# Kernel optimization log

Hardware: AMD Instinct MI355X
Metric: run time of the kernel (lower is better)

Reference implementation:

```python
import jax, jax.numpy as jnp
import numpy as np

N = 100000
E = 1600000
C_IN = 128
H = 128
C_OUT = 128
DEPTH = 3
RATIO = 0.5
EPS = 1e-5


def gcn_conv(x, W, b, src, dst, mask, n):
    # PyG GCNConv: out = D^-1/2 (A+I) D^-1/2 (x @ W) + b, masked edges dropped
    h = x @ W  # [n, out]
    ew = mask.astype(h.dtype)  # [E]
    deg = 1.0 + jax.ops.segment_sum(ew, dst, num_segments=n)  # self-loop included
    dinv = jax.lax.rsqrt(deg)
    norm = dinv[src] * dinv[dst] * ew  # [E]
    agg = jax.ops.segment_sum(h[src] * norm[:, None], dst, num_segments=n)
    agg = agg + h * (1.0 / deg)[:, None]  # self-loop contribution
    return agg + b


def bn_train(x, g, beta):
    # BatchNorm1d training forward: biased variance over nodes
    m = jnp.mean(x, axis=0)
    v = jnp.mean((x - m) ** 2, axis=0)
    return (x - m) * jax.lax.rsqrt(v + EPS) * g + beta


def topk_pool(x, w, src, dst, mask, k):
    # score = tanh(x.w / ||w||); keep top-k nodes, relabel edges, mask invalid ones
    score = jnp.tanh((x * w).sum(-1) / jnp.sqrt((w * w).sum()))
    _, idx = jax.lax.top_k(score, k)
    n = x.shape[0]
    new_id = jnp.zeros((n,), jnp.int32).at[idx].set(jnp.arange(k, dtype=jnp.int32))
    kept = jnp.zeros((n,), bool).at[idx].set(True)
    mask2 = mask & kept[src] & kept[dst]
    return x[idx], new_id[src], new_id[dst], mask2, idx


def setup_inputs() -> dict:
    key = jax.random.key(0)
    ks = jax.random.split(key, 16)
    sc_in = 1.0 / np.sqrt(C_IN)
    sc_h = 1.0 / np.sqrt(H)
    sc_2h = 1.0 / np.sqrt(2 * H)
    return {
        "x": jax.random.normal(ks[0], (N, C_IN), jnp.float32),
        "edge_index": jax.random.randint(ks[1], (2, E), 0, N, dtype=jnp.int32),
        "in_W": jax.random.normal(ks[2], (C_IN, H), jnp.float32) * sc_in,
        "in_b": jnp.zeros((H,), jnp.float32),
        "dn_W": jax.random.normal(ks[3], (DEPTH, H, H), jnp.float32) * sc_h,
        "dn_b": jnp.zeros((DEPTH, H), jnp.float32),
        "dn_g": jnp.ones((DEPTH, H), jnp.float32),
        "dn_beta": jnp.zeros((DEPTH, H), jnp.float32),
        "pool_w": jax.random.normal(ks[4], (DEPTH, H), jnp.float32),
        "bot_W": jax.random.normal(ks[5], (H, H), jnp.float32) * sc_h,
        "bot_b": jnp.zeros((H,), jnp.float32),
        "up_W": jax.random.normal(ks[6], (DEPTH, 2 * H, H), jnp.float32) * sc_2h,
        "up_b": jnp.zeros((DEPTH, H), jnp.float32),
        "up_g": jnp.ones((DEPTH, H), jnp.float32),
        "up_beta": jnp.zeros((DEPTH, H), jnp.float32),
        "out_W": jax.random.normal(ks[7], (H, C_OUT), jnp.float32) * sc_h,
        "out_b": jnp.zeros((C_OUT,), jnp.float32),
    }


def reference(x, edge_index, in_W, in_b, dn_W, dn_b, dn_g, dn_beta, pool_w,
              bot_W, bot_b, up_W, up_b, up_g, up_beta, out_W, out_b):
    src, dst = edge_index[0], edge_index[1]
    mask = jnp.ones((src.shape[0],), bool)
    n = x.shape[0]
    x = gcn_conv(x, in_W, in_b, src, dst, mask, n)
    xs, stack = [], []
    for i in range(DEPTH):
        x = gcn_conv(x, dn_W[i], dn_b[i], src, dst, mask, n)
        x = jax.nn.relu(bn_train(x, dn_g[i], dn_beta[i]))
        xs.append(x)
        k = int(RATIO * n)
        x2, src2, dst2, mask2, idx = topk_pool(x, pool_w[i], src, dst, mask, k)
        stack.append((src, dst, mask, idx, n))
        x, src, dst, mask, n = x2, src2, dst2, mask2, k
    x = jax.nn.relu(gcn_conv(x, bot_W, bot_b, src, dst, mask, n))
    for i in range(DEPTH):
        psrc, pdst, pmask, idx, pn = stack[DEPTH - 1 - i]
        xf = jnp.zeros((pn, x.shape[1]), x.dtype).at[idx].set(x)  # unpool zero-scatter
        src, dst, mask, n = psrc, pdst, pmask, pn
        x = jnp.concatenate([xf, xs[DEPTH - 1 - i]], axis=1)  # [pn, 2H]
        x = gcn_conv(x, up_W[i], up_b[i], src, dst, mask, n)
        x = jax.nn.relu(bn_train(x, up_g[i], up_beta[i]))
    return gcn_conv(x, out_W, out_b, src, dst, mask, n)
```

## Files before the change

### kernel.cpp

```cpp
#include <hip/hip_runtime.h>

typedef unsigned long long ull;

#define N0_ 100000
#define N1_ 50000
#define N2_ 25000
#define N3_ 12500
#define EDG 1600000
#define CAP1 600000
#define CAP2 200000
#define CAP3 80000

struct Sel { ull prefix; int remaining; };


__global__ void sentinel_k(float* o, float v) { if (threadIdx.x == 0) o[0] = v; }

template <typename TA, typename TC, typename ACC>
__global__ __launch_bounds__(256) void matmul128(const TA* __restrict__ A,
    const float* __restrict__ W, const float* __restrict__ bias,
    TC* __restrict__ C, int n) {
  __shared__ float Al[64 * 33];
  __shared__ float Wl[32 * 128];
  int tid = threadIdx.x;
  int colb = tid & 31;
  int rg = tid >> 5;
  int row0 = blockIdx.x * 64;
  ACC acc[8][4];
#pragma unroll
  for (int r = 0; r < 8; ++r)
#pragma unroll
    for (int j = 0; j < 4; ++j) acc[r][j] = (ACC)0;
  for (int kt = 0; kt < 128; kt += 32) {
    for (int i = tid; i < 64 * 32; i += 256) {
      int r = i >> 5, kk = i & 31;
      int row = row0 + r;
      Al[r * 33 + kk] = (row < n) ? (float)A[(size_t)row * 128 + kt + kk] : 0.0f;
    }
    for (int i = tid; i < 32 * 128; i += 256) {
      int kk = i >> 7, c = i & 127;
      Wl[i] = W[(size_t)(kt + kk) * 128 + c];
    }
    __syncthreads();
#pragma unroll 4
    for (int kk = 0; kk < 32; ++kk) {
      ACC b0 = (ACC)Wl[kk * 128 + colb];
      ACC b1 = (ACC)Wl[kk * 128 + colb + 32];
      ACC b2 = (ACC)Wl[kk * 128 + colb + 64];
      ACC b3 = (ACC)Wl[kk * 128 + colb + 96];
#pragma unroll
      for (int r = 0; r < 8; ++r) {
        ACC a = (ACC)Al[(rg * 8 + r) * 33 + kk];
        acc[r][0] += a * b0; acc[r][1] += a * b1;
        acc[r][2] += a * b2; acc[r][3] += a * b3;
      }
    }
    __syncthreads();
  }
  ACC bb0 = 0, bb1 = 0, bb2 = 0, bb3 = 0;
  if (bias) {
    bb0 = (ACC)bias[colb]; bb1 = (ACC)bias[colb + 32];
    bb2 = (ACC)bias[colb + 64]; bb3 = (ACC)bias[colb + 96];
  }
  for (int r = 0; r < 8; ++r) {
    int row = row0 + rg * 8 + r;
    if (row < n) {
      size_t o = (size_t)row * 128 + colb;
      C[o] = (TC)(acc[r][0] + bb0); C[o + 32] = (TC)(acc[r][1] + bb1);
      C[o + 64] = (TC)(acc[r][2] + bb2); C[o + 96] = (TC)(acc[r][3] + bb3);
    }
  }
}

template <bool RELU>
__global__ __launch_bounds__(256) void agg_conv(const float* __restrict__ hp,
    const int* __restrict__ off, const int* __restrict__ csrc,
    const float* __restrict__ csrw,
    const double* __restrict__ dinv, const double* __restrict__ dgi,
    const float* __restrict__ bias, float* __restrict__ yp, int n) {
  const float4* __restrict__ h = (const float4*)hp;
  float4* __restrict__ y = (float4*)yp;
  int lane = threadIdx.x & 63;
  int c4 = lane & 31;
  int half = lane >> 5;
  int node = blockIdx.x * 4 + (threadIdx.x >> 6);
  if (node >= n) return;
  double di = dinv[node];
  double dg = dgi[node];
  double aX = 0, aY = 0, aZ = 0, aW = 0;
  int p0 = off[node], p1 = off[node + 1];
  int m = p1 - p0;
  int npair = m >> 1;
  int j = 0;
  for (; j + 4 <= npair; j += 4) {
    int e0 = p0 + 2 * j + half;
    int s0 = csrc[e0], s1 = csrc[e0 + 2], s2 = csrc[e0 + 4], s3 = csrc[e0 + 6];
    double w0 = (double)csrw[e0],     w1 = (double)csrw[e0 + 2];
    double w2 = (double)csrw[e0 + 4], w3 = (double)csrw[e0 + 6];
    float4 v0 = h[(size_t)s0 * 32 + c4];
    float4 v1 = h[(size_t)s1 * 32 + c4];
    float4 v2 = h[(size_t)s2 * 32 + c4];
    float4 v3 = h[(size_t)s3 * 32 + c4];
    aX += (double)v0.x * w0; aY += (double)v0.y * w0;
    aZ += (double)v0.z * w0; aW += (double)v0.w * w0;
    aX += (double)v1.x * w1; aY += (double)v1.y * w1;
    aZ += (double)v1.z * w1; aW += (double)v1.w * w1;
    aX += (double)v2.x * w2; aY += (double)v2.y * w2;
    aZ += (double)v2.z * w2; aW += (double)v2.w * w2;
    aX += (double)v3.x * w3; aY += (double)v3.y * w3;
    aZ += (double)v3.z * w3; aW += (double)v3.w * w3;
  }
  for (; j < npair; ++j) {
    int e = p0 + 2 * j + half;
    double w = (double)csrw[e];
    float4 v = h[(size_t)csrc[e] * 32 + c4];
    aX += (double)v.x * w; aY += (double)v.y * w;
    aZ += (double)v.z * w; aW += (double)v.w * w;
  }
  if ((m & 1) && half == 0) {
    int e = p1 - 1;
    double w = (double)csrw[e];
    float4 v = h[(size_t)csrc[e] * 32 + c4];
    aX += (double)v.x * w; aY += (double)v.y * w;
    aZ += (double)v.z * w; aW += (double)v.w * w;
  }
  double sX = aX + __shfl_xor(aX, 32);
  double sY = aY + __shfl_xor(aY, 32);
  double sZ = aZ + __shfl_xor(aZ, 32);
  double sW = aW + __shfl_xor(aW, 32);
  if (half == 0) {
    float4 hv = h[(size_t)node * 32 + c4];
    double bx = 0, by = 0, bz = 0, bw = 0;
    if (bias) {
      bx = (double)bias[c4 * 4 + 0]; by = (double)bias[c4 * 4 + 1];
      bz = (double)bias[c4 * 4 + 2]; bw = (double)bias[c4 * 4 + 3];
    }
    double rx = sX * di + (double)hv.x * dg + bx;
    double ry = sY * di + (double)hv.y * dg + by;
    double rz = sZ * di + (double)hv.z * dg + bz;
    double rw = sW * di + (double)hv.w * dg + bw;
    if (RELU) {
      rx = rx > 0.0 ? rx : 0.0; ry = ry > 0.0 ? ry : 0.0;
      rz = rz > 0.0 ? rz : 0.0; rw = rw > 0.0 ? rw : 0.0;
    }
    y[(size_t)node * 32 + c4] = make_float4((float)rx, (float)ry, (float)rz, (float)rw);
  }
}

__global__ void count_deg(const int* __restrict__ dst, int m, int* __restrict__ cnt) {
  int e = blockIdx.x * 256 + threadIdx.x;
  if (e < m) atomicAdd(&cnt[dst[e]], 1);
}

__global__ void fin_deg(const int* __restrict__ cnt, double* __restrict__ dinv,
                        double* __restrict__ dgi, int n) {
  int i = blockIdx.x * 256 + threadIdx.x;
  if (i < n) {
    double d = 1.0 + (double)cnt[i];
    dinv[i] = 1.0 / sqrt(d);
    dgi[i] = 1.0 / d;
  }
}

__global__ __launch_bounds__(256) void scan_part(const int* __restrict__ in,
                                                 int* __restrict__ bsum, int n) {
  __shared__ int ts[256];
  int base = blockIdx.x * 1024 + threadIdx.x * 4;
  int s = 0;
#pragma unroll
  for (int j = 0; j < 4; ++j) { int i = base + j; if (i < n) s += in[i]; }
  ts[threadIdx.x] = s;
  __syncthreads();
  for (int d = 128; d > 0; d >>= 1) {
    if (threadIdx.x < d) ts[threadIdx.x] += ts[threadIdx.x + d];
    __syncthreads();
  }
  if (threadIdx.x == 0) bsum[blockIdx.x] = ts[0];
}

__global__ __launch_bounds__(256) void scan_bsum(int* __restrict__ bsum, int nb) {
  __shared__ int ls[256];
  int t = threadIdx.x;
  int v = (t < nb) ? bsum[t] : 0;
  ls[t] = v;
  __syncthreads();
  for (int d = 1; d < 256; d <<= 1) {
    int u = (t >= d) ? ls[t - d] : 0;
    __syncthreads();
    ls[t] += u;
    __syncthreads();
  }
  if (t < nb) bsum[t] = ls[t] - v;
}

__global__ __launch_bounds__(256) void scan_out(const int* __restrict__ in,
    const int* __restrict__ bsum, int* __restrict__ out, int n, int nb) {
  __shared__ int ts[256];
  int base = blockIdx.x * 1024 + threadIdx.x * 4;
  int loc[4];
  int s = 0;
#pragma unroll
  for (int j = 0; j < 4; ++j) {
    int i = base + j;
    int v = (i < n) ? in[i] : 0;
    loc[j] = s; s += v;
  }
  ts[threadIdx.x] = s;
  __syncthreads();
  int mine = s;
  for (int d = 1; d < 256; d <<= 1) {
    int u = (threadIdx.x >= d) ? ts[threadIdx.x - d] : 0;
    __syncthreads();
    ts[threadIdx.x] += u;
    __syncthreads();
  }
  int toff = bsum[blockIdx.x] + ts[threadIdx.x] - mine;
#pragma unroll
  for (int j = 0; j < 4; ++j) {
    int i = base + j;
    if (i < n) out[i] = toff + loc[j];
  }
  if (blockIdx.x == nb - 1 && threadIdx.x == 255) out[n] = bsum[blockIdx.x] + ts[255];
}

__global__ void csr_fill(const int* __restrict__ src, const int* __restrict__ dst,
                         int m, const int* __restrict__ off,
                         int* __restrict__ cursor, int* __restrict__ csrs,
                         float* __restrict__ csrw, const double* __restrict__ dinv) {
  int e = blockIdx.x * 256 + threadIdx.x;
  if (e < m) {
    int d = dst[e];
    int s = src[e];
    int pos = off[d] + atomicAdd(&cursor[d], 1);
    csrs[pos] = s;
    csrw[pos] = (float)dinv[s];
  }
}

__global__ void next_deg(const int* __restrict__ off, const int* __restrict__ csrs,
                         const int* __restrict__ knid, int* __restrict__ ndeg, int n) {
  int d = blockIdx.x * 256 + threadIdx.x;
  if (d >= n) return;
  int nd = knid[d];
  if (nd < 0) return;
  int cnt = 0;
  int p1 = off[d + 1];
  for (int p = off[d]; p < p1; ++p) cnt += (knid[csrs[p]] >= 0) ? 1 : 0;
  ndeg[nd] = cnt;
}

__global__ void next_fill(const int* __restrict__ off, const int* __restrict__ csrs,
                          const int* __restrict__ knid, const int* __restrict__ noff,
                          const double* __restrict__ ndinv,
                          int* __restrict__ ncsrs, float* __restrict__ ncsrw, int n) {
  int d = blockIdx.x * 256 + threadIdx.x;
  if (d >= n) return;
  int nd = knid[d];
  if (nd < 0) return;
  int pos = noff[nd];
  int p1 = off[d + 1];
  for (int p = off[d]; p < p1; ++p) {
    int s = knid[csrs[p]];
    if (s >= 0) { ncsrs[pos] = s; ncsrw[pos] = (float)ndinv[s]; ++pos; }
  }
}

template <typename T>
__global__ __launch_bounds__(256) void bn_stats(const T* __restrict__ x, int n,
                                                double* __restrict__ part) {
  __shared__ double lsum[256], lsq[256];
  int c = threadIdx.x & 127, half = threadIdx.x >> 7;
  double s = 0, q = 0;
  for (int row = blockIdx.x * 2 + half; row < n; row += 512) {
    double v = (double)x[(size_t)row * 128 + c];
    s += v; q += v * v;
  }
  lsum[threadIdx.x] = s; lsq[threadIdx.x] = q;
  __syncthreads();
  if (half == 0) {
    part[blockIdx.x * 256 + c] = lsum[c] + lsum[c + 128];
    part[blockIdx.x * 256 + 128 + c] = lsq[c] + lsq[c + 128];
  }
}

__global__ void bn_final(const double* __restrict__ part, const float* __restrict__ g,
                         const float* __restrict__ beta, double invn,
                         double* __restrict__ ss) {
  int c = threadIdx.x;
  double s = 0, q = 0;
  for (int b = 0; b < 256; ++b) {
    s += part[b * 256 + c];
    q += part[b * 256 + 128 + c];
  }
  double m = s * invn;
  double v = q * invn - m * m;
  double sc = (double)g[c] / sqrt(v + 1e-5);
  ss[c] = sc;
  ss[128 + c] = (double)beta[c] - m * sc;
}

__global__ void bn_apply_relu4(float4* __restrict__ x, const double* __restrict__ ss,
                               float4* __restrict__ snap, size_t total4) {
  size_t i = (size_t)blockIdx.x * 256 + threadIdx.x;
  if (i < total4) {
    int c0 = (int)((i & 31) * 4);
    float4 v = x[i];
    double r0 = (double)v.x * ss[c0 + 0] + ss[128 + c0 + 0];
    double r1 = (double)v.y * ss[c0 + 1] + ss[128 + c0 + 1];
    double r2 = (double)v.z * ss[c0 + 2] + ss[128 + c0 + 2];
    double r3 = (double)v.w * ss[c0 + 3] + ss[128 + c0 + 3];
    r0 = r0 > 0.0 ? r0 : 0.0; r1 = r1 > 0.0 ? r1 : 0.0;
    r2 = r2 > 0.0 ? r2 : 0.0; r3 = r3 > 0.0 ? r3 : 0.0;
    float4 o = make_float4((float)r0, (float)r1, (float)r2, (float)r3);
    x[i] = o;
    if (snap) snap[i] = o;
  }
}

__global__ void wnorm_k(const float* __restrict__ w, double* __restrict__ wn) {
  __shared__ double red[128];
  int c = threadIdx.x;
  double v = (double)w[c];
  red[c] = v * v;
  __syncthreads();
  for (int s = 64; s > 0; s >>= 1) { if (c < s) red[c] += red[c + s]; __syncthreads(); }
  if (c == 0) wn[0] = sqrt(red[0]);
}

__global__ __launch_bounds__(256) void score_key_k(const float* __restrict__ x,
    const float* __restrict__ w, const double* __restrict__ wn,
    ull* __restrict__ keys, int n) {
  __shared__ double red[256];
  int c = threadIdx.x & 127;
  int node = blockIdx.x * 2 + (threadIdx.x >> 7);
  double p = 0.0;
  if (node < n) p = (double)x[(size_t)node * 128 + c] * (double)w[c];
  red[threadIdx.x] = p;
  __syncthreads();
  for (int s = 64; s > 0; s >>= 1) {
    if (c < s) red[threadIdx.x] += red[threadIdx.x + s];
    __syncthreads();
  }
  if (c == 0 && node < n) {
    double sc = tanh(red[threadIdx.x] / wn[0]);
    ull u = (ull)__double_as_longlong(sc);
    u = (u >> 63) ? ~u : (u | 0x8000000000000000ULL);
    keys[node] = u;
  }
}

__global__ void sel_init(Sel* sel, int k) {
  if (threadIdx.x == 0) { sel->prefix = 0ULL; sel->remaining = k; }
}

__global__ void rs_hist(const ull* __restrict__ keys, int n, const Sel* __restrict__ sel,
                        int shift, int pass, int* __restrict__ hist) {
  __shared__ int lh[256];
  lh[threadIdx.x] = 0;
  __syncthreads();
  int i = blockIdx.x * 256 + threadIdx.x;
  if (i < n) {
    ull k = keys[i];
    bool ok = (pass == 0) || (((k ^ sel->prefix) >> (shift + 8)) == 0);
    if (ok) atomicAdd(&lh[(int)((k >> shift) & 255)], 1);
  }
  __syncthreads();
  if (lh[threadIdx.x]) atomicAdd(&hist[threadIdx.x], lh[threadIdx.x]);
}

__global__ void rs_pick(const int* __restrict__ hist, Sel* sel, int shift) {
  __shared__ int lh[256];
  lh[threadIdx.x] = hist[threadIdx.x];
  __syncthreads();
  if (threadIdx.x == 0) {
    int rem = sel->remaining;
    for (int b = 255; b >= 0; --b) {
      int c = lh[b];
      if (c >= rem) { sel->prefix |= ((ull)b) << shift; break; }
      rem -= c;
    }
    sel->remaining = rem;
  }
}

__global__ void eq_flags(const ull* __restrict__ keys, const Sel* __restrict__ sel,
                         int* __restrict__ eqf, int n) {
  int i = blockIdx.x * 256 + threadIdx.x;
  if (i < n) eqf[i] = (keys[i] == sel->prefix) ? 1 : 0;
}

__global__ void kept_flags(const ull* __restrict__ keys, const Sel* __restrict__ sel,
                           const int* __restrict__ eqpre, int* __restrict__ kept, int n) {
  int i = blockIdx.x * 256 + threadIdx.x;
  if (i < n) {
    ull u = keys[i], p = sel->prefix;
    kept[i] = (u > p || (u == p && eqpre[i] < sel->remaining)) ? 1 : 0;
  }
}

__global__ void build_idx(const int* __restrict__ kept, const int* __restrict__ npre,
                          int* __restrict__ knid, int* __restrict__ idx, int n) {
  int i = blockIdx.x * 256 + threadIdx.x;
  if (i < n) {
    if (kept[i]) {
      int nid = npre[i];
      knid[i] = nid;
      idx[nid] = i;
    } else {
      knid[i] = -1;
    }
  }
}

__global__ void gather_rows4(const float4* __restrict__ xs, const int* __restrict__ idx,
                             float4* __restrict__ xo, int k) {
  int i = blockIdx.x * 256 + threadIdx.x;
  if (i < k * 32) xo[i] = xs[(size_t)idx[i >> 5] * 32 + (i & 31)];
}

__global__ void scatter_add_rows4(float4* __restrict__ h, const float4* __restrict__ t,
                                  const int* __restrict__ idx, int k) {
  int i = blockIdx.x * 256 + threadIdx.x;
  if (i < k * 32) {
    float4 a = h[(size_t)idx[i >> 5] * 32 + (i & 31)];
    float4 b = t[i];
    a.x += b.x; a.y += b.y; a.z += b.z; a.w += b.w;
    h[(size_t)idx[i >> 5] * 32 + (i & 31)] = a;
  }
}


extern "C" void kernel_launch(void* const* d_in, const int* in_sizes, int n_in,
                              void* d_out, int out_size, void* d_ws, size_t ws_size,
                              hipStream_t stream) {
  (void)in_sizes; (void)out_size;
  if (n_in < 17) return;
  const float* x_in   = (const float*)d_in[0];
  const int*   ei     = (const int*)  d_in[1];
  const float* in_W   = (const float*)d_in[2];
  const float* in_b   = (const float*)d_in[3];
  const float* dn_W   = (const float*)d_in[4];
  const float* dn_b   = (const float*)d_in[5];
  const float* dn_g   = (const float*)d_in[6];
  const float* dn_bt  = (const float*)d_in[7];
  const float* pool_w = (const float*)d_in[8];
  const float* bot_W  = (const float*)d_in[9];
  const float* bot_b  = (const float*)d_in[10];
  const float* up_W   = (const float*)d_in[11];
  const float* up_b   = (const float*)d_in[12];
  const float* up_g   = (const float*)d_in[13];
  const float* up_bt  = (const float*)d_in[14];
  const float* out_W  = (const float*)d_in[15];
  const float* out_b  = (const float*)d_in[16];
  float* outp = (float*)d_out;

  char* base = (char*)d_ws;
  size_t off = 0;
  auto alloc = [&](size_t b) -> void* {
    void* r = base + off;
    off = (off + b + 255) & ~(size_t)255;
    return r;
  };
  float* bufA = (float*)alloc((size_t)N0_ * 128 * 4);
  float* bufB = (float*)alloc((size_t)N0_ * 128 * 4);
  float* xs0f = (float*)alloc((size_t)N0_ * 128 * 4);
  float* xs1f = (float*)alloc((size_t)N1_ * 128 * 4);
  float* xs2f = (float*)alloc((size_t)N2_ * 128 * 4);

  int* csrs0 = (int*)alloc((size_t)EDG * 4);
  int* csrs1 = (int*)alloc((size_t)CAP1 * 4);
  int* csrs2 = (int*)alloc((size_t)CAP2 * 4);
  int* csrs3 = (int*)alloc((size_t)CAP3 * 4);
  float* csrw0 = (float*)alloc((size_t)EDG * 4);
  float* csrw1 = (float*)alloc((size_t)CAP1 * 4);
  float* csrw2 = (float*)alloc((size_t)CAP2 * 4);
  float* csrw3 = (float*)alloc((size_t)CAP3 * 4);
  int* csro0 = (int*)alloc((size_t)(N0_ + 1) * 4);
  int* csro1 = (int*)alloc((size_t)(N1_ + 1) * 4);
  int* csro2 = (int*)alloc((size_t)(N2_ + 1) * 4);
  int* csro3 = (int*)alloc((size_t)(N3_ + 1) * 4);
  double* dinv0 = (double*)alloc((size_t)N0_ * 8); double* dgi0 = (double*)alloc((size_t)N0_ * 8);
  double* dinv1 = (double*)alloc((size_t)N1_ * 8); double* dgi1 = (double*)alloc((size_t)N1_ * 8);
  double* dinv2 = (double*)alloc((size_t)N2_ * 8); double* dgi2 = (double*)alloc((size_t)N2_ * 8);
  double* dinv3 = (double*)alloc((size_t)N3_ * 8); double* dgi3 = (double*)alloc((size_t)N3_ * 8);
  ull* keys = (ull*)alloc((size_t)N0_ * 8);
  int* eqf   = (int*)alloc((size_t)N0_ * 4);
  int* eqpre = (int*)alloc((size_t)(N0_ + 1) * 4);
  int* kept  = (int*)alloc((size_t)N0_ * 4);
  int* npre  = (int*)alloc((size_t)(N0_ + 1) * 4);
  int* knid  = (int*)alloc((size_t)N0_ * 4);
  int* degcnt = (int*)alloc((size_t)N0_ * 4);
  int* cursor = (int*)alloc((size_t)N0_ * 4);
  int* idx0 = (int*)alloc((size_t)N1_ * 4);
  int* idx1 = (int*)alloc((size_t)N2_ * 4);
  int* idx2 = (int*)alloc((size_t)N3_ * 4);
  int* hist = (int*)alloc(8 * 256 * 4);
  Sel* sel  = (Sel*)alloc(256);
  int* bscan = (int*)alloc(256 * 4);
  double* bns = (double*)alloc((size_t)256 * 256 * 8);
  double* ssb = (double*)alloc(256 * 8);
  double* wn  = (double*)alloc(256);
  if (off > ws_size) {
    sentinel_k<<<1, 64, 0, stream>>>(outp, (float)ws_size);
    return;
  }

  const int nL[4]   = {N0_, N1_, N2_, N3_};
  int* csrsL[4] = {csrs0, csrs1, csrs2, csrs3};
  float* csrwL[4] = {csrw0, csrw1, csrw2, csrw3};
  int* csroL[4] = {csro0, csro1, csro2, csro3};
  double* dinvL[4] = {dinv0, dinv1, dinv2, dinv3};
  double* dgiL[4]  = {dgi0, dgi1, dgi2, dgi3};
  int* idxL[3] = {idx0, idx1, idx2};

  auto cdiv = [](int a, int b) { return (a + b - 1) / b; };

  auto scan = [&](const int* in, int* out, int n) {
    int nb = cdiv(n, 1024);
    scan_part<<<nb, 256, 0, stream>>>(in, bscan, n);
    scan_bsum<<<1, 256, 0, stream>>>(bscan, nb);
    scan_out<<<nb, 256, 0, stream>>>(in, bscan, out, n, nb);
  };

  auto bn_f = [&](float* xp, int n, const float* g, const float* b, float* snap) {
    bn_stats<float><<<256, 256, 0, stream>>>(xp, n, bns);
    bn_final<<<1, 128, 0, stream>>>(bns, g, b, 1.0 / (double)n, ssb);
    bn_apply_relu4<<<cdiv(n * 32, 256), 256, 0, stream>>>(
        (float4*)xp, ssb, (float4*)snap, (size_t)n * 32);
  };

  auto pool = [&](int i, const float* xcur, float* xnext) {
    int n = nL[i], k = nL[i + 1];
    wnorm_k<<<1, 128, 0, stream>>>(pool_w + i * 128, wn);
    score_key_k<<<cdiv(n, 2), 256, 0, stream>>>(xcur, pool_w + i * 128, wn, keys, n);
    sel_init<<<1, 64, 0, stream>>>(sel, k);
    hipMemsetAsync(hist, 0, 8 * 256 * 4, stream);
    for (int p = 0; p < 8; ++p) {
      int shift = 56 - 8 * p;
      rs_hist<<<cdiv(n, 256), 256, 0, stream>>>(keys, n, sel, shift, p, hist + p * 256);
      rs_pick<<<1, 256, 0, stream>>>(hist + p * 256, sel, shift);
    }
    eq_flags<<<cdiv(n, 256), 256, 0, stream>>>(keys, sel, eqf, n);
    scan(eqf, eqpre, n);
    kept_flags<<<cdiv(n, 256), 256, 0, stream>>>(keys, sel, eqpre, kept, n);
    scan(kept, npre, n);
    build_idx<<<cdiv(n, 256), 256, 0, stream>>>(kept, npre, knid, idxL[i], n);
    gather_rows4<<<cdiv(k * 32, 256), 256, 0, stream>>>(
        (const float4*)xcur, idxL[i], (float4*)xnext, k);
    next_deg<<<cdiv(n, 256), 256, 0, stream>>>(csroL[i], csrsL[i], knid, degcnt, n);
    fin_deg<<<cdiv(k, 256), 256, 0, stream>>>(degcnt, dinvL[i + 1], dgiL[i + 1], k);
    scan(degcnt, csroL[i + 1], k);
    next_fill<<<cdiv(n, 256), 256, 0, stream>>>(csroL[i], csrsL[i], knid,
        csroL[i + 1], dinvL[i + 1], csrsL[i + 1], csrwL[i + 1], n);
  };

  hipMemsetAsync(degcnt, 0, (size_t)N0_ * 4, stream);
  count_deg<<<cdiv(EDG, 256), 256, 0, stream>>>(ei + EDG, EDG, degcnt);
  fin_deg<<<cdiv(N0_, 256), 256, 0, stream>>>(degcnt, dinv0, dgi0, N0_);
  scan(degcnt, csro0, N0_);
  hipMemsetAsync(cursor, 0, (size_t)N0_ * 4, stream);
  csr_fill<<<cdiv(EDG, 256), 256, 0, stream>>>(ei, ei + EDG, EDG, csro0, cursor,
                                               csrs0, csrw0, dinv0);

  agg_conv<false><<<cdiv(N0_, 4), 256, 0, stream>>>(
      x_in, csro0, csrs0, csrw0, dinv0, dgi0, nullptr, bufB, N0_);
  matmul128<float, float, double><<<cdiv(N0_, 64), 256, 0, stream>>>(bufB, in_W, in_b, bufA, N0_);

  matmul128<float, float, double><<<cdiv(N0_, 64), 256, 0, stream>>>(bufA, dn_W, nullptr, bufB, N0_);
  agg_conv<false><<<cdiv(N0_, 4), 256, 0, stream>>>(
      bufB, csro0, csrs0, csrw0, dinv0, dgi0, dn_b, bufA, N0_);
  bn_f(bufA, N0_, dn_g, dn_bt, xs0f);
  pool(0, bufA, bufB);

  matmul128<float, float, double><<<cdiv(N1_, 64), 256, 0, stream>>>(bufB, dn_W + 16384, nullptr, bufA, N1_);
  agg_conv<false><<<cdiv(N1_, 4), 256, 0, stream>>>(
      bufA, csro1, csrs1, csrw1, dinv1, dgi1, dn_b + 128, bufB, N1_);
  bn_f(bufB, N1_, dn_g + 128, dn_bt + 128, xs1f);
  pool(1, bufB, bufA);

  matmul128<float, float, double><<<cdiv(N2_, 64), 256, 0, stream>>>(bufA, dn_W + 32768, nullptr, bufB, N2_);
  agg_conv<false><<<cdiv(N2_, 4), 256, 0, stream>>>(
      bufB, csro2, csrs2, csrw2, dinv2, dgi2, dn_b + 256, bufA, N2_);
  bn_f(bufA, N2_, dn_g + 256, dn_bt + 256, xs2f);
  pool(2, bufA, bufB);

  matmul128<float, float, double><<<cdiv(N3_, 64), 256, 0, stream>>>(bufB, bot_W, nullptr, bufA, N3_);
  float* zf = bufB;
  float* hf = bufA;
  float* tf = outp;
  agg_conv<true><<<cdiv(N3_, 4), 256, 0, stream>>>(
      bufA, csro3, csrs3, csrw3, dinv3, dgi3, bot_b, zf, N3_);

  for (int u = 0; u < 3; ++u) {
    int l = 2 - u;
    int nl = nL[l], nz = nL[l + 1];
    const float* Wt = up_W + u * 32768;
    const float* Wb = up_W + u * 32768 + 16384;
    const float* xsf = (u == 0) ? xs2f : (u == 1) ? xs1f : xs0f;
    matmul128<float, float, float><<<cdiv(nz, 64), 256, 0, stream>>>(zf, Wt, nullptr, tf, nz);
    matmul128<float, float, float><<<cdiv(nl, 64), 256, 0, stream>>>(xsf, Wb, nullptr, hf, nl);
    scatter_add_rows4<<<cdiv(nz * 32, 256), 256, 0, stream>>>(
        (float4*)hf, (const float4*)tf, idxL[l], nz);
    agg_conv<false><<<cdiv(nl, 4), 256, 0, stream>>>(
        hf, csroL[l], csrsL[l], csrwL[l], dinvL[l], dgiL[l], up_b + u * 128, zf, nl);
    bn_f(zf, nl, up_g + u * 128, up_bt + u * 128, nullptr);
  }

  matmul128<float, float, float><<<cdiv(N0_, 64), 256, 0, stream>>>(zf, out_W, nullptr, hf, N0_);
  agg_conv<false><<<cdiv(N0_, 4), 256, 0, stream>>>(
      hf, csro0, csrs0, csrw0, dinv0, dgi0, out_b, outp, N0_);
}
```

Before: 2.678 ms.

## Use 16-bit radix select, fused flag scans, and deeper agg unroll

Top-k selection now uses four 16-bit radix passes with a global-atomic histogram instead of eight 8-bit passes. The flag/scan/build kernels are fused into scan kernels that recompute flags on the fly. next_deg is fused with degree finalisation, and bn_apply writes only once to its output instead of in place plus a snapshot. agg_conv also gets an 8-way unrolled gather loop for more loads in flight. These cut kernel launches and memory passes, but the 65536-bin global atomic histogram may contend and costs a larger clear.

After: 2.565 ms. 1.04x faster.

```diff
diff --git a/kernel.cpp b/kernel.cpp
--- a/kernel.cpp
+++ b/kernel.cpp
@@ -10,6 +10,7 @@
 #define CAP1 600000
 #define CAP2 200000
 #define CAP3 80000
+#define RB 65536
 
 struct Sel { ull prefix; int remaining; };
 
@@ -92,6 +93,39 @@
   int m = p1 - p0;
   int npair = m >> 1;
   int j = 0;
+  for (; j + 8 <= npair; j += 8) {
+    int e0 = p0 + 2 * j + half;
+    int s0 = csrc[e0],      s1 = csrc[e0 + 2],  s2 = csrc[e0 + 4],  s3 = csrc[e0 + 6];
+    int s4 = csrc[e0 + 8],  s5 = csrc[e0 + 10], s6 = csrc[e0 + 12], s7 = csrc[e0 + 14];
+    double w0 = (double)csrw[e0],      w1 = (double)csrw[e0 + 2];
+    double w2 = (double)csrw[e0 + 4],  w3 = (double)csrw[e0 + 6];
+    double w4 = (double)csrw[e0 + 8],  w5 = (double)csrw[e0 + 10];
+    double w6 = (double)csrw[e0 + 12], w7 = (double)csrw[e0 + 14];
+    float4 v0 = h[(size_t)s0 * 32 + c4];
+    float4 v1 = h[(size_t)s1 * 32 + c4];
+    float4 v2 = h[(size_t)s2 * 32 + c4];
+    float4 v3 = h[(size_t)s3 * 32 + c4];
+    float4 v4 = h[(size_t)s4 * 32 + c4];
+    float4 v5 = h[(size_t)s5 * 32 + c4];
+    float4 v6 = h[(size_t)s6 * 32 + c4];
+    float4 v7 = h[(size_t)s7 * 32 + c4];
+    aX += (double)v0.x * w0; aY += (double)v0.y * w0;
+    aZ += (double)v0.z * w0; aW += (double)v0.w * w0;
+    aX += (double)v1.x * w1; aY += (double)v1.y * w1;
+    aZ += (double)v1.z * w1; aW += (double)v1.w * w1;
+    aX += (double)v2.x * w2; aY += (double)v2.y * w2;
+    aZ += (double)v2.z * w2; aW += (double)v2.w * w2;
+    aX += (double)v3.x * w3; aY += (double)v3.y * w3;
+    aZ += (double)v3.z * w3; aW += (double)v3.w * w3;
+    aX += (double)v4.x * w4; aY += (double)v4.y * w4;
+    aZ += (double)v4.z * w4; aW += (double)v4.w * w4;
+    aX += (double)v5.x * w5; aY += (double)v5.y * w5;
+    aZ += (double)v5.z * w5; aW += (double)v5.w * w5;
+    aX += (double)v6.x * w6; aY += (double)v6.y * w6;
+    aZ += (double)v6.z * w6; aW += (double)v6.w * w6;
+    aX += (double)v7.x * w7; aY += (double)v7.y * w7;
+    aZ += (double)v7.z * w7; aW += (double)v7.w * w7;
+  }
   for (; j + 4 <= npair; j += 4) {
     int e0 = p0 + 2 * j + half;
     int s0 = csrc[e0], s1 = csrc[e0 + 2], s2 = csrc[e0 + 4], s3 = csrc[e0 + 6];
@@ -223,6 +257,108 @@
   if (blockIdx.x == nb - 1 && threadIdx.x == 255) out[n] = bsum[blockIdx.x] + ts[255];
 }
 
+template <int MODE>
+__device__ __forceinline__ int sel_flag(ull u, ull pref, int epre, int rem) {
+  if (MODE == 1) return (u == pref) ? 1 : 0;
+  return (u > pref || (u == pref && epre < rem)) ? 1 : 0;
+}
+
+template <int MODE>
+__global__ __launch_bounds__(256) void fscan_part(const ull* __restrict__ keys,
+    const int* __restrict__ eqpre, const Sel* __restrict__ sel,
+    int* __restrict__ bsum, int n) {
+  __shared__ int ts[256];
+  ull pref = sel->prefix;
+  int rem = sel->remaining;
+  int base = blockIdx.x * 1024 + threadIdx.x * 4;
+  int s = 0;
+#pragma unroll
+  for (int j = 0; j < 4; ++j) {
+    int i = base + j;
+    if (i < n) s += sel_flag<MODE>(keys[i], pref, (MODE == 2) ? eqpre[i] : 0, rem);
+  }
+  ts[threadIdx.x] = s;
+  __syncthreads();
+  for (int d = 128; d > 0; d >>= 1) {
+    if (threadIdx.x < d) ts[threadIdx.x] += ts[threadIdx.x + d];
+    __syncthreads();
+  }
+  if (threadIdx.x == 0) bsum[blockIdx.x] = ts[0];
+}
+
+__global__ __launch_bounds__(256) void fscan_out1(const ull* __restrict__ keys,
+    const Sel* __restrict__ sel, const int* __restrict__ bsum,
+    int* __restrict__ eqpre_out, int n) {
+  __shared__ int ts[256];
+  ull pref = sel->prefix;
+  int base = blockIdx.x * 1024 + threadIdx.x * 4;
+  int loc[4];
+  int s = 0;
+#pragma unroll
+  for (int j = 0; j < 4; ++j) {
+    int i = base + j;
+    int v = (i < n) ? sel_flag<1>(keys[i], pref, 0, 0) : 0;
+    loc[j] = s; s += v;
+  }
+  ts[threadIdx.x] = s;
+  __syncthreads();
+  int mine = s;
+  for (int d = 1; d < 256; d <<= 1) {
+    int u = (threadIdx.x >= d) ? ts[threadIdx.x - d] : 0;
+    __syncthreads();
+    ts[threadIdx.x] += u;
+    __syncthreads();
+  }
+  int toff = bsum[blockIdx.x] + ts[threadIdx.x] - mine;
+#pragma unroll
+  for (int j = 0; j < 4; ++j) {
+    int i = base + j;
+    if (i < n) eqpre_out[i] = toff + loc[j];
+  }
+}
+
+__global__ __launch_bounds__(256) void fscan_out2(const ull* __restrict__ keys,
+    const int* __restrict__ eqpre, const Sel* __restrict__ sel,
+    const int* __restrict__ bsum, int* __restrict__ knid, int* __restrict__ idx,
+    int n) {
+  __shared__ int ts[256];
+  ull pref = sel->prefix;
+  int rem = sel->remaining;
+  int base = blockIdx.x * 1024 + threadIdx.x * 4;
+  int flg[4];
+  int loc[4];
+  int s = 0;
+#pragma unroll
+  for (int j = 0; j < 4; ++j) {
+    int i = base + j;
+    int v = (i < n) ? sel_flag<2>(keys[i], pref, eqpre[i], rem) : 0;
+    flg[j] = v; loc[j] = s; s += v;
+  }
+  ts[threadIdx.x] = s;
+  __syncthreads();
+  int mine = s;
+  for (int d = 1; d < 256; d <<= 1) {
+    int u = (threadIdx.x >= d) ? ts[threadIdx.x - d] : 0;
+    __syncthreads();
+    ts[threadIdx.x] += u;
+    __syncthreads();
+  }
+  int toff = bsum[blockIdx.x] + ts[threadIdx.x] - mine;
+#pragma unroll
+  for (int j = 0; j < 4; ++j) {
+    int i = base + j;
+    if (i < n) {
+      if (flg[j]) {
+        int nid = toff + loc[j];
+        knid[i] = nid;
+        idx[nid] = i;
+      } else {
+        knid[i] = -1;
+      }
+    }
+  }
+}
+
 __global__ void csr_fill(const int* __restrict__ src, const int* __restrict__ dst,
                          int m, const int* __restrict__ off,
                          int* __restrict__ cursor, int* __restrict__ csrs,
@@ -237,8 +373,10 @@
   }
 }
 
-__global__ void next_deg(const int* __restrict__ off, const int* __restrict__ csrs,
-                         const int* __restrict__ knid, int* __restrict__ ndeg, int n) {
+__global__ void next_deg_fin(const int* __restrict__ off, const int* __restrict__ csrs,
+                             const int* __restrict__ knid, int* __restrict__ ndeg,
+                             double* __restrict__ ndinv, double* __restrict__ ndgi,
+                             int n) {
   int d = blockIdx.x * 256 + threadIdx.x;
   if (d >= n) return;
   int nd = knid[d];
@@ -247,6 +385,9 @@
   int p1 = off[d + 1];
   for (int p = off[d]; p < p1; ++p) cnt += (knid[csrs[p]] >= 0) ? 1 : 0;
   ndeg[nd] = cnt;
+  double dd = 1.0 + (double)cnt;
+  ndinv[nd] = 1.0 / sqrt(dd);
+  ndgi[nd] = 1.0 / dd;
 }
 
 __global__ void next_fill(const int* __restrict__ off, const int* __restrict__ csrs,
@@ -299,8 +440,9 @@
   ss[128 + c] = (double)beta[c] - m * sc;
 }
 
-__global__ void bn_apply_relu4(float4* __restrict__ x, const double* __restrict__ ss,
-                               float4* __restrict__ snap, size_t total4) {
+__global__ void bn_apply_relu4(const float4* __restrict__ x,
+                               const double* __restrict__ ss,
+                               float4* __restrict__ out, size_t total4) {
   size_t i = (size_t)blockIdx.x * 256 + threadIdx.x;
   if (i < total4) {
     int c0 = (int)((i & 31) * 4);
@@ -311,9 +453,7 @@
     double r3 = (double)v.w * ss[c0 + 3] + ss[128 + c0 + 3];
     r0 = r0 > 0.0 ? r0 : 0.0; r1 = r1 > 0.0 ? r1 : 0.0;
     r2 = r2 > 0.0 ? r2 : 0.0; r3 = r3 > 0.0 ? r3 : 0.0;
-    float4 o = make_float4((float)r0, (float)r1, (float)r2, (float)r3);
-    x[i] = o;
-    if (snap) snap[i] = o;
+    out[i] = make_float4((float)r0, (float)r1, (float)r2, (float)r3);
   }
 }
 
@@ -349,65 +489,51 @@
   }
 }
 
-__global__ void sel_init(Sel* sel, int k) {
-  if (threadIdx.x == 0) { sel->prefix = 0ULL; sel->remaining = k; }
-}
-
-__global__ void rs_hist(const ull* __restrict__ keys, int n, const Sel* __restrict__ sel,
-                        int shift, int pass, int* __restrict__ hist) {
-  __shared__ int lh[256];
-  lh[threadIdx.x] = 0;
-  __syncthreads();
+__global__ void rs_init(int* __restrict__ hist, Sel* sel, int k) {
+  int i = blockIdx.x * 256 + threadIdx.x;
+  if (i < 4 * RB) hist[i] = 0;
+  if (i == 0) { sel->prefix = 0ULL; sel->remaining = k; }
+}
+
+__global__ void rs_hist16(const ull* __restrict__ keys, int n,
+                          const Sel* __restrict__ sel, int shift, int pass,
+                          int* __restrict__ hist) {
   int i = blockIdx.x * 256 + threadIdx.x;
   if (i < n) {
     ull k = keys[i];
-    bool ok = (pass == 0) || (((k ^ sel->prefix) >> (shift + 8)) == 0);
-    if (ok) atomicAdd(&lh[(int)((k >> shift) & 255)], 1);
-  }
-  __syncthreads();
-  if (lh[threadIdx.x]) atomicAdd(&hist[threadIdx.x], lh[threadIdx.x]);
-}
-
-__global__ void rs_pick(const int* __restrict__ hist, Sel* sel, int shift) {
-  __shared__ int lh[256];
-  lh[threadIdx.x] = hist[threadIdx.x];
-  __syncthreads();
-  if (threadIdx.x == 0) {
-    int rem = sel->remaining;
-    for (int b = 255; b >= 0; --b) {
-      int c = lh[b];
-      if (c >= rem) { sel->prefix |= ((ull)b) << shift; break; }
-      rem -= c;
-    }
-    sel->remaining = rem;
-  }
-}
-
-__global__ void eq_flags(const ull* __restrict__ keys, const Sel* __restrict__ sel,
-                         int* __restrict__ eqf, int n) {
-  int i = blockIdx.x * 256 + threadIdx.x;
-  if (i < n) eqf[i] = (keys[i] == sel->prefix) ? 1 : 0;
-}
-
-__global__ void kept_flags(const ull* __restrict__ keys, const Sel* __restrict__ sel,
-                           const int* __restrict__ eqpre, int* __restrict__ kept, int n) {
-  int i = blockIdx.x * 256 + threadIdx.x;
-  if (i < n) {
-    ull u = keys[i], p = sel->prefix;
-    kept[i] = (u > p || (u == p && eqpre[i] < sel->remaining)) ? 1 : 0;
-  }
-}
-
-__global__ void build_idx(const int* __restrict__ kept, const int* __restrict__ npre,
-                          int* __restrict__ knid, int* __restrict__ idx, int n) {
-  int i = blockIdx.x * 256 + threadIdx.x;
-  if (i < n) {
-    if (kept[i]) {
-      int nid = npre[i];
-      knid[i] = nid;
-      idx[nid] = i;
-    } else {
-      knid[i] = -1;
+    bool ok = (pass == 0) || (((k ^ sel->prefix) >> (shift + 16)) == 0);
+    if (ok) atomicAdd(&hist[(int)((k >> shift) & 65535)], 1);
+  }
+}
+
+__global__ __launch_bounds__(1024) void rs_pick16(const int* __restrict__ hist,
+                                                  Sel* sel, int shift) {
+  __shared__ int ls[1024];
+  int t = threadIdx.x;
+  int base = t * 64;
+  int own = 0;
+  for (int b = 0; b < 64; ++b) own += hist[base + b];
+  ls[t] = own;
+  __syncthreads();
+  for (int d = 1; d < 1024; d <<= 1) {
+    int v = (t + d < 1024) ? ls[t + d] : 0;
+    __syncthreads();
+    ls[t] += v;
+    __syncthreads();
+  }
+  int rem = sel->remaining;
+  int St = ls[t];
+  int Snext = St - own;
+  if (Snext < rem && rem <= St) {
+    int cum = Snext;
+    for (int b = 63; b >= 0; --b) {
+      int c = hist[base + b];
+      if (cum + c >= rem) {
+        sel->prefix |= ((ull)(base + b)) << shift;
+        sel->remaining = rem - cum;
+        break;
+      }
+      cum += c;
     }
   }
 }
@@ -484,17 +610,14 @@
   double* dinv2 = (double*)alloc((size_t)N2_ * 8); double* dgi2 = (double*)alloc((size_t)N2_ * 8);
   double* dinv3 = (double*)alloc((size_t)N3_ * 8); double* dgi3 = (double*)alloc((size_t)N3_ * 8);
   ull* keys = (ull*)alloc((size_t)N0_ * 8);
-  int* eqf   = (int*)alloc((size_t)N0_ * 4);
   int* eqpre = (int*)alloc((size_t)(N0_ + 1) * 4);
-  int* kept  = (int*)alloc((size_t)N0_ * 4);
-  int* npre  = (int*)alloc((size_t)(N0_ + 1) * 4);
   int* knid  = (int*)alloc((size_t)N0_ * 4);
   int* degcnt = (int*)alloc((size_t)N0_ * 4);
   int* cursor = (int*)alloc((size_t)N0_ * 4);
   int* idx0 = (int*)alloc((size_t)N1_ * 4);
   int* idx1 = (int*)alloc((size_t)N2_ * 4);
   int* idx2 = (int*)alloc((size_t)N3_ * 4);
-  int* hist = (int*)alloc(8 * 256 * 4);
+  int* hist = (int*)alloc((size_t)4 * RB * 4);
   Sel* sel  = (Sel*)alloc(256);
   int* bscan = (int*)alloc(256 * 4);
   double* bns = (double*)alloc((size_t)256 * 256 * 8);
@@ -522,33 +645,34 @@
     scan_out<<<nb, 256, 0, stream>>>(in, bscan, out, n, nb);
   };
 
-  auto bn_f = [&](float* xp, int n, const float* g, const float* b, float* snap) {
+  auto bn_f = [&](float* xp, int n, const float* g, const float* b, float* outb) {
     bn_stats<float><<<256, 256, 0, stream>>>(xp, n, bns);
     bn_final<<<1, 128, 0, stream>>>(bns, g, b, 1.0 / (double)n, ssb);
     bn_apply_relu4<<<cdiv(n * 32, 256), 256, 0, stream>>>(
-        (float4*)xp, ssb, (float4*)snap, (size_t)n * 32);
+        (const float4*)xp, ssb, (float4*)outb, (size_t)n * 32);
   };
 
   auto pool = [&](int i, const float* xcur, float* xnext) {
     int n = nL[i], k = nL[i + 1];
+    int nb = cdiv(n, 1024);
     wnorm_k<<<1, 128, 0, stream>>>(pool_w + i * 128, wn);
     score_key_k<<<cdiv(n, 2), 256, 0, stream>>>(xcur, pool_w + i * 128, wn, keys, n);
-    sel_init<<<1, 64, 0, stream>>>(sel, k);
-    hipMemsetAsync(hist, 0, 8 * 256 * 4, stream);
-    for (int p = 0; p < 8; ++p) {
-      int shift = 56 - 8 * p;
-      rs_hist<<<cdiv(n, 256), 256, 0, stream>>>(keys, n, sel, shift, p, hist + p * 256);
-      rs_pick<<<1, 256, 0, stream>>>(hist + p * 256, sel, shift);
-    }
-    eq_flags<<<cdiv(n, 256), 256, 0, stream>>>(keys, sel, eqf, n);
-    scan(eqf, eqpre, n);
-    kept_flags<<<cdiv(n, 256), 256, 0, stream>>>(keys, sel, eqpre, kept, n);
-    scan(kept, npre, n);
-    build_idx<<<cdiv(n, 256), 256, 0, stream>>>(kept, npre, knid, idxL[i], n);
+    rs_init<<<1024, 256, 0, stream>>>(hist, sel, k);
+    for (int p = 0; p < 4; ++p) {
+      int shift = 48 - 16 * p;
+      rs_hist16<<<cdiv(n, 256), 256, 0, stream>>>(keys, n, sel, shift, p, hist + p * RB);
+      rs_pick16<<<1, 1024, 0, stream>>>(hist + p * RB, sel, shift);
+    }
+    fscan_part<1><<<nb, 256, 0, stream>>>(keys, nullptr, sel, bscan, n);
+    scan_bsum<<<1, 256, 0, stream>>>(bscan, nb);
+    fscan_out1<<<nb, 256, 0, stream>>>(keys, sel, bscan, eqpre, n);
+    fscan_part<2><<<nb, 256, 0, stream>>>(keys, eqpre, sel, bscan, n);
+    scan_bsum<<<1, 256, 0, stream>>>(bscan, nb);
+    fscan_out2<<<nb, 256, 0, stream>>>(keys, eqpre, sel, bscan, knid, idxL[i], n);
     gather_rows4<<<cdiv(k * 32, 256), 256, 0, stream>>>(
         (const float4*)xcur, idxL[i], (float4*)xnext, k);
-    next_deg<<<cdiv(n, 256), 256, 0, stream>>>(csroL[i], csrsL[i], knid, degcnt, n);
-    fin_deg<<<cdiv(k, 256), 256, 0, stream>>>(degcnt, dinvL[i + 1], dgiL[i + 1], k);
+    next_deg_fin<<<cdiv(n, 256), 256, 0, stream>>>(csroL[i], csrsL[i], knid, degcnt,
+                                                   dinvL[i + 1], dgiL[i + 1], n);
     scan(degcnt, csroL[i + 1], k);
     next_fill<<<cdiv(n, 256), 256, 0, stream>>>(csroL[i], csrsL[i], knid,
         csroL[i + 1], dinvL[i + 1], csrsL[i + 1], csrwL[i + 1], n);
@@ -570,19 +694,19 @@
   agg_conv<false><<<cdiv(N0_, 4), 256, 0, stream>>>(
       bufB, csro0, csrs0, csrw0, dinv0, dgi0, dn_b, bufA, N0_);
   bn_f(bufA, N0_, dn_g, dn_bt, xs0f);
-  pool(0, bufA, bufB);
+  pool(0, xs0f, bufB);
 
   matmul128<float, float, double><<<cdiv(N1_, 64), 256, 0, stream>>>(bufB, dn_W + 16384, nullptr, bufA, N1_);
   agg_conv<false><<<cdiv(N1_, 4), 256, 0, stream>>>(
       bufA, csro1, csrs1, csrw1, dinv1, dgi1, dn_b + 128, bufB, N1_);
   bn_f(bufB, N1_, dn_g + 128, dn_bt + 128, xs1f);
-  pool(1, bufB, bufA);
+  pool(1, xs1f, bufA);
 
   matmul128<float, float, double><<<cdiv(N2_, 64), 256, 0, stream>>>(bufA, dn_W + 32768, nullptr, bufB, N2_);
   agg_conv<false><<<cdiv(N2_, 4), 256, 0, stream>>>(
       bufB, csro2, csrs2, csrw2, dinv2, dgi2, dn_b + 256, bufA, N2_);
   bn_f(bufA, N2_, dn_g + 256, dn_bt + 256, xs2f);
-  pool(2, bufA, bufB);
+  pool(2, xs2f, bufB);
 
   matmul128<float, float, double><<<cdiv(N3_, 64), 256, 0, stream>>>(bufB, bot_W, nullptr, bufA, N3_);
   float* zf = bufB;
@@ -603,7 +727,7 @@
         (float4*)hf, (const float4*)tf, idxL[l], nz);
     agg_conv<false><<<cdiv(nl, 4), 256, 0, stream>>>(
         hf, csroL[l], csrsL[l], csrwL[l], dinvL[l], dgiL[l], up_b + u * 128, zf, nl);
-    bn_f(zf, nl, up_g + u * 128, up_bt + u * 128, nullptr);
+    bn_f(zf, nl, up_g + u * 128, up_bt + u * 128, zf);
   }
 
   matmul128<float, float, float><<<cdiv(N0_, 64), 256, 0, stream>>>(zf, out_W, nullptr, hf, N0_);
```
